# Performance work log

Hardware: AMD Instinct MI355X
Metric: run time of the kernel (lower is better)

## Reference

```python
import jax, jax.numpy as jnp
import numpy as np

NEG = -10000.0
SLOPE = 0.2


def setup_inputs() -> dict:
    key = jax.random.key(0)
    k1, k2, k3, k4, k5 = jax.random.split(key, 5)
    B, N, F_in, F_out = 8, 2048, 512, 512
    text = jax.random.normal(k1, (B, N, F_in), dtype=jnp.float32)
    adj = jax.random.randint(k2, (B, N, N), 0, 2, dtype=jnp.int32)
    sc = 1.0 / np.sqrt(F_in)
    W = jax.random.normal(k3, (F_in, F_out), dtype=jnp.float32) * sc
    b = jnp.zeros((F_out,), dtype=jnp.float32)
    a_src = jax.random.normal(k4, (F_out,), dtype=jnp.float32) * sc
    a_dst = jax.random.normal(k5, (F_out,), dtype=jnp.float32) * sc
    return {"text": text, "adj": adj, "W": W, "b": b, "a_src": a_src, "a_dst": a_dst}


def reference(text, adj, W, b, a_src, a_dst):
    # hidden: [B, N, F_out]
    hidden = jnp.einsum("bnf,fo->bno", text, W) + b
    s = jnp.einsum("bno,o->bn", hidden, a_src)  # src score per node
    d = jnp.einsum("bno,o->bn", hidden, a_dst)  # dst score per node
    scores = s[:, :, None] + d[:, None, :]      # [B, N, N]
    scores = jnp.where(scores >= 0, scores, SLOPE * scores)  # LeakyReLU
    # faithful to original: masked_fill where adj.bool() is True
    scores = jnp.where(adj.astype(bool), NEG, scores)
    attn = jax.nn.softmax(scores, axis=-1)
    return jnp.einsum("bnm,bmo->bno", attn, hidden)
```

## Files before the change

### kernel.cpp

```cpp
#include <hip/hip_runtime.h>
#include <stdint.h>

#define NB 8
#define NN 2048
#define NF 512
#define TOTN (NB * NN)

typedef unsigned short u16;
typedef short bf16x8 __attribute__((ext_vector_type(8)));
typedef float f32x4 __attribute__((ext_vector_type(4)));

__device__ __forceinline__ u16 f2bf(float x) {
  unsigned u = __float_as_uint(x);
  unsigned r = 0x7FFFu + ((u >> 16) & 1u);
  return (u16)((u + r) >> 16);
}

__device__ __forceinline__ void gl2lds16(const void* g, void* l) {
  __builtin_amdgcn_global_load_lds((const __attribute__((address_space(1))) void*)g,
                                   (__attribute__((address_space(3))) void*)l,
                                   16, 0, 0);
}


__global__ __launch_bounds__(256) void prep_kernel(
    const float* __restrict__ text, const float* __restrict__ W,
    const int* __restrict__ adj, u16* __restrict__ text_bf,
    u16* __restrict__ Wt, uint32_t* __restrict__ bm,
    float* __restrict__ sd) {
  int blk = blockIdx.x;
  if (blk < 8192) {
    int idx = blk * 256 + threadIdx.x;
    float4 v = ((const float4*)text)[idx];
    ushort4 o;
    o.x = f2bf(v.x); o.y = f2bf(v.y); o.z = f2bf(v.z); o.w = f2bf(v.w);
    ((ushort4*)text_bf)[idx] = o;
  } else if (blk < 9216) {
    int t = (blk - 8192) * 256 + threadIdx.x;
    int o = t >> 9, f = t & 511;
    Wt[o * NF + f] = f2bf(W[f * NF + o]);
  } else if (blk < 13312) {
    int gid = (blk - 9216) * 256 + threadIdx.x;
    const int4* p = (const int4*)(adj + (size_t)gid * 32);
    uint32_t bits = 0;
#pragma unroll
    for (int c = 0; c < 8; ++c) {
      int4 a = p[c];
      bits |= (uint32_t)(a.x != 0) << (c * 4 + 0);
      bits |= (uint32_t)(a.y != 0) << (c * 4 + 1);
      bits |= (uint32_t)(a.z != 0) << (c * 4 + 2);
      bits |= (uint32_t)(a.w != 0) << (c * 4 + 3);
    }
    bm[gid] = bits;
  } else {
    float4* p = (float4*)sd;
#pragma unroll
    for (int c = 0; c < 32; ++c)
      p[c * 256 + threadIdx.x] = (float4){0.f, 0.f, 0.f, 0.f};
  }
}

__global__ __launch_bounds__(256) void gemm1_kernel(
    const u16* __restrict__ A,
    const u16* __restrict__ Bt,
    const float* __restrict__ bias, const float* __restrict__ a_src,
    const float* __restrict__ a_dst, u16* __restrict__ hS,
    float* __restrict__ s, float* __restrict__ d) {
  __shared__ u16 Alds[128 * 32];
  __shared__ u16 Blds[128 * 32];

  const int bn = blockIdx.x, bm_ = blockIdx.y;
  const int t = threadIdx.x, wave = t >> 6, lane = t & 63;
  const int wm = (wave >> 1) * 64, wn = (wave & 1) * 64;

  f32x4 acc[4][4];
#pragma unroll
  for (int i = 0; i < 4; ++i)
#pragma unroll
    for (int j = 0; j < 4; ++j) acc[i][j] = (f32x4){0.f, 0.f, 0.f, 0.f};

  const int rowA0 = bm_ * 128, rowB0 = bn * 128;
  const int srow = (lane >> 2);
  const int scol = (lane & 3) * 8;

  for (int kt = 0; kt < NF; kt += 32) {
#pragma unroll
    for (int q = 0; q < 2; ++q) {
      int r = wave * 32 + q * 16;
      gl2lds16(A + (size_t)(rowA0 + r + srow) * NF + (kt + scol), &Alds[r * 32]);
    }
#pragma unroll
    for (int q = 0; q < 2; ++q) {
      int r = wave * 32 + q * 16;
      gl2lds16(Bt + (size_t)(rowB0 + r + srow) * NF + (kt + scol), &Blds[r * 32]);
    }
    __syncthreads();

    const int fr = lane & 15;
    const int k0 = (lane >> 4) * 8;
    bf16x8 af[4], bfr[4];
#pragma unroll
    for (int i = 0; i < 4; ++i)
      af[i] = *(const bf16x8*)&Alds[(wm + i * 16 + fr) * 32 + k0];
#pragma unroll
    for (int j = 0; j < 4; ++j)
      bfr[j] = *(const bf16x8*)&Blds[(wn + j * 16 + fr) * 32 + k0];
#pragma unroll
    for (int i = 0; i < 4; ++i)
#pragma unroll
      for (int j = 0; j < 4; ++j)
        acc[i][j] = __builtin_amdgcn_mfma_f32_16x16x32_bf16(af[i], bfr[j],
                                                            acc[i][j], 0, 0, 0);
    __syncthreads();
  }

  const int quad = lane >> 4, ln16 = lane & 15;
  float sa[4] = {0.f, 0.f, 0.f, 0.f}, da[4] = {0.f, 0.f, 0.f, 0.f};
#pragma unroll
  for (int i = 0; i < 4; ++i) {
    int m0 = bm_ * 128 + wm + i * 16 + quad * 4;
#pragma unroll
    for (int r = 0; r < 4; ++r) {
      int m = m0 + r;
      float bv = bias[m];
      float asv = a_src[m], adv = a_dst[m];
      int oh = m >> 8, och = (m >> 4) & 15, rc = m & 15;
#pragma unroll
      for (int j = 0; j < 4; ++j) {
        int n = bn * 128 + wn + j * 16 + ln16;
        float h = acc[i][j][r] + bv;
        int zz = n >> 11, nz = n & 2047;
        int kc = nz >> 5, kin = nz & 31;
        size_t off = ((((size_t)zz * 2 + oh) * 64 + kc) << 13)
                     + (och << 9)
                     + ((size_t)(rc * 4 + ((kin >> 3) ^ ((rc >> 1) & 3))) << 3)
                     + (kin & 7);
        hS[off] = f2bf(h);
        sa[j] = fmaf(h, asv, sa[j]);
        da[j] = fmaf(h, adv, da[j]);
      }
    }
  }
#pragma unroll
  for (int j = 0; j < 4; ++j) {
    float v = sa[j] + __shfl_xor(sa[j], 16, 64);
    v += __shfl_xor(v, 32, 64);
    float w2 = da[j] + __shfl_xor(da[j], 16, 64);
    w2 += __shfl_xor(w2, 32, 64);
    if (quad == 0) {
      int n = bn * 128 + wn + j * 16 + ln16;
      atomicAdd(&s[n], v);
      atomicAdd(&d[n], w2);
    }
  }
}

__global__ __launch_bounds__(256, 2) void fused_attn_kernel(
    const uint32_t* __restrict__ bm, const float* __restrict__ s,
    const float* __restrict__ d, const u16* __restrict__ hS,
    float* __restrict__ out) {
  __shared__ u16 Blds[2][16384];
  __shared__ u16 Plds[4096];
  __shared__ float lpart[256];
  __shared__ float linv_lds[64];

  const int z = blockIdx.z, oh = blockIdx.y;
  const int i0 = blockIdx.x * 64;
  const int t = threadIdx.x, wave = t >> 6, lane = t & 63;
  const int quad = lane >> 4, ln16 = lane & 15;

  const int pr = t >> 2;
  const int ko = (t & 3) * 16;
  const float si = s[z * NN + i0 + pr];
  const uint32_t* bmrow = bm + (size_t)(z * NN + i0 + pr) * 64;
  const float* db = d + z * NN;

  const char* slabB = (const char*)hS + (size_t)(z * 2 + oh) * 1048576;

  f32x4 acc[4][4];
#pragma unroll
  for (int i = 0; i < 4; ++i)
#pragma unroll
    for (int j = 0; j < 4; ++j) acc[i][j] = (f32x4){0.f, 0.f, 0.f, 0.f};

  const int fslot = ln16 * 4 + (quad ^ ((ln16 >> 1) & 3));
  const int prc = pr & 15, pch = pr >> 4;
  const int ph = ko >> 5, pq0 = (ko >> 3) & 3;
  char* pbase = (char*)Plds + ph * 4096 + pch * 1024;
  char* pdst0 = pbase + (prc * 4 + (pq0 ^ ((prc >> 1) & 3))) * 16;
  char* pdst1 = pbase + (prc * 4 + ((pq0 + 1) ^ ((prc >> 1) & 3))) * 16;

  uint32_t bw = bmrow[ko >> 5];
  float4 dv[4];
#pragma unroll
  for (int c = 0; c < 4; ++c) dv[c] = *(const float4*)&db[ko + c * 4];
  __builtin_amdgcn_sched_barrier(0);
#pragma unroll
  for (int c = 0; c < 8; ++c) {
    int boff = (c * 4 + wave) * 1024;
    gl2lds16(slabB + boff + lane * 16, (char*)&Blds[0][0] + boff);
  }

  float lsum = 0.f;
  int buf = 0;

  for (int kt = 0; kt < NN; kt += 64) {
    uint32_t bits16 = (bw >> (ko & 16)) & 0xFFFFu;
    u16 pk[16];
#pragma unroll
    for (int cc = 0; cc < 4; ++cc) {
      float4 dq = dv[cc];
#pragma unroll
      for (int e = 0; e < 4; ++e) {
        float dj = (e == 0) ? dq.x : (e == 1) ? dq.y : (e == 2) ? dq.z : dq.w;
        float x = si + dj;
        float xm = fmaxf(x, 0.2f * x);
        float p = ((bits16 >> (cc * 4 + e)) & 1u) ? 0.f : __expf(xm);
        lsum += p;
        pk[cc * 4 + e] = f2bf(p);
      }
    }

    bool more = (kt + 64 < NN);
    if (more) {
      bw = bmrow[((kt + 64) >> 5) + (ko >> 5)];
#pragma unroll
      for (int c = 0; c < 4; ++c)
        dv[c] = *(const float4*)&db[kt + 64 + ko + c * 4];
      __builtin_amdgcn_sched_barrier(0);
      const char* gB = slabB + (size_t)(kt + 64) * 512;
      char* bdst = (char*)&Blds[buf ^ 1][0];
#pragma unroll
      for (int c = 0; c < 8; ++c) {
        int boff = (c * 4 + wave) * 1024;
        gl2lds16(gB + boff + lane * 16, bdst + boff);
      }
    }

    *(int4*)pdst0 = *(int4*)&pk[0];
    *(int4*)pdst1 = *(int4*)&pk[8];

    if (more)
      asm volatile("s_waitcnt vmcnt(13) lgkmcnt(0)" ::: "memory");
    else
      asm volatile("s_waitcnt vmcnt(0) lgkmcnt(0)" ::: "memory");
    __builtin_amdgcn_s_barrier();
    asm volatile("" ::: "memory");

    const char* bbase = (const char*)&Blds[buf][0];
#pragma unroll
    for (int h = 0; h < 2; ++h) {
      bf16x8 af[4], bfv[4];
#pragma unroll
      for (int i = 0; i < 4; ++i)
        af[i] = *(const bf16x8*)((const char*)Plds + h * 4096 + i * 1024 + fslot * 16);
#pragma unroll
      for (int j = 0; j < 4; ++j)
        bfv[j] = *(const bf16x8*)(bbase + h * 16384 +
                                  (wave * 4 + j) * 1024 + fslot * 16);
#pragma unroll
      for (int i = 0; i < 4; ++i)
#pragma unroll
        for (int j = 0; j < 4; ++j)
          acc[i][j] = __builtin_amdgcn_mfma_f32_16x16x32_bf16(af[i], bfv[j],
                                                              acc[i][j], 0, 0, 0);
    }

    asm volatile("" ::: "memory");
    __builtin_amdgcn_s_barrier();
    asm volatile("" ::: "memory");
    buf ^= 1;
  }

  lpart[pr * 4 + (t & 3)] = lsum;
  __syncthreads();
  if (t < 64) {
    const float* lp = &lpart[t * 4];
    linv_lds[t] = 1.0f / ((lp[0] + lp[1]) + (lp[2] + lp[3]));
  }
  __syncthreads();

#pragma unroll
  for (int i = 0; i < 4; ++i) {
#pragma unroll
    for (int r = 0; r < 4; ++r) {
      int m = i * 16 + quad * 4 + r;
      float sc = linv_lds[m];
      float* ob = out + ((size_t)(z * NN) + i0 + m) * NF + oh * 256 + wave * 64;
#pragma unroll
      for (int j = 0; j < 4; ++j) ob[j * 16 + ln16] = acc[i][j][r] * sc;
    }
  }
}

extern "C" void kernel_launch(void* const* d_in, const int* in_sizes, int n_in,
                              void* d_out, int out_size, void* d_ws,
                              size_t ws_size, hipStream_t stream) {
  const float* text  = (const float*)d_in[0];
  const int*   adj   = (const int*)d_in[1];
  const float* W     = (const float*)d_in[2];
  const float* bias  = (const float*)d_in[3];
  const float* a_src = (const float*)d_in[4];
  const float* a_dst = (const float*)d_in[5];
  float* out = (float*)d_out;

  char* ws = (char*)d_ws;
  u16*      text_bf = (u16*)(ws + 0);
  u16*      Wt      = (u16*)(ws + 16777216);
  u16*      hS      = (u16*)(ws + 17301504);
  float*    s       = (float*)(ws + 34078720);
  float*    d       = (float*)(ws + 34144256);
  uint32_t* bmask   = (uint32_t*)(ws + 34209792);

  prep_kernel<<<13313, 256, 0, stream>>>(text, W, adj, text_bf, Wt, bmask, s);

  gemm1_kernel<<<dim3(128, 4, 1), 256, 0, stream>>>(Wt, text_bf, bias, a_src,
                                                    a_dst, hS, s, d);

  fused_attn_kernel<<<dim3(NN / 64, 2, NB), 256, 0, stream>>>(bmask, s, d, hS,
                                                              out);
}
```

Baseline: 299.0 us.

## Move adjacency bitmask packing into GEMM launch and reorder attention block mapping

Adjacency-to-bitmask packing moves from the prep kernel into extra blocks of the GEMM kernel, so the memory-bound adj read (128MB) can overlap with the compute-bound GEMM tiles instead of running serially before it. The attention kernel switches to a 1D grid whose lowest bits index the batch and output half. Consecutive blocks therefore hit different batches, which changes L2/MALL locality and the spread across XCDs. The GEMM blocks come first in the 1D grid, so the packing blocks may only fill in after them.

```diff
diff --git a/kernel.cpp b/kernel.cpp
--- a/kernel.cpp
+++ b/kernel.cpp
@@ -25,8 +25,7 @@
 
 __global__ __launch_bounds__(256) void prep_kernel(
     const float* __restrict__ text, const float* __restrict__ W,
-    const int* __restrict__ adj, u16* __restrict__ text_bf,
-    u16* __restrict__ Wt, uint32_t* __restrict__ bm,
+    u16* __restrict__ text_bf, u16* __restrict__ Wt,
     float* __restrict__ sd) {
   int blk = blockIdx.x;
   if (blk < 8192) {
@@ -39,8 +38,29 @@
     int t = (blk - 8192) * 256 + threadIdx.x;
     int o = t >> 9, f = t & 511;
     Wt[o * NF + f] = f2bf(W[f * NF + o]);
-  } else if (blk < 13312) {
-    int gid = (blk - 9216) * 256 + threadIdx.x;
+  } else {
+    float4* p = (float4*)sd;
+#pragma unroll
+    for (int c = 0; c < 32; ++c)
+      p[c * 256 + threadIdx.x] = (float4){0.f, 0.f, 0.f, 0.f};
+  }
+}
+
+__global__ __launch_bounds__(256) void gemm1_kernel(
+    const u16* __restrict__ A,
+    const u16* __restrict__ Bt,
+    const float* __restrict__ bias, const float* __restrict__ a_src,
+    const float* __restrict__ a_dst, const int* __restrict__ adj,
+    u16* __restrict__ hS, float* __restrict__ s, float* __restrict__ d,
+    uint32_t* __restrict__ bmout) {
+  __shared__ u16 Alds[128 * 32];
+  __shared__ u16 Blds[128 * 32];
+
+  const int bid = blockIdx.x;
+  const int t = threadIdx.x;
+
+  if (bid >= 512) {
+    int gid = (bid - 512) * 256 + t;
     const int4* p = (const int4*)(adj + (size_t)gid * 32);
     uint32_t bits = 0;
 #pragma unroll
@@ -51,26 +71,12 @@
       bits |= (uint32_t)(a.z != 0) << (c * 4 + 2);
       bits |= (uint32_t)(a.w != 0) << (c * 4 + 3);
     }
-    bm[gid] = bits;
-  } else {
-    float4* p = (float4*)sd;
-#pragma unroll
-    for (int c = 0; c < 32; ++c)
-      p[c * 256 + threadIdx.x] = (float4){0.f, 0.f, 0.f, 0.f};
-  }
-}
-
-__global__ __launch_bounds__(256) void gemm1_kernel(
-    const u16* __restrict__ A,
-    const u16* __restrict__ Bt,
-    const float* __restrict__ bias, const float* __restrict__ a_src,
-    const float* __restrict__ a_dst, u16* __restrict__ hS,
-    float* __restrict__ s, float* __restrict__ d) {
-  __shared__ u16 Alds[128 * 32];
-  __shared__ u16 Blds[128 * 32];
-
-  const int bn = blockIdx.x, bm_ = blockIdx.y;
-  const int t = threadIdx.x, wave = t >> 6, lane = t & 63;
+    bmout[gid] = bits;
+    return;
+  }
+
+  const int bn = bid & 127, bm_ = bid >> 7;
+  const int wave = t >> 6, lane = t & 63;
   const int wm = (wave >> 1) * 64, wn = (wave & 1) * 64;
 
   f32x4 acc[4][4];
@@ -164,8 +170,10 @@
   __shared__ float lpart[256];
   __shared__ float linv_lds[64];
 
-  const int z = blockIdx.z, oh = blockIdx.y;
-  const int i0 = blockIdx.x * 64;
+  const int bid = blockIdx.x;
+  const int z = bid & 7;
+  const int oh = (bid >> 3) & 1;
+  const int i0 = (bid >> 4) * 64;
   const int t = threadIdx.x, wave = t >> 6, lane = t & 63;
   const int quad = lane >> 4, ln16 = lane & 15;
 
@@ -312,11 +320,10 @@
   float*    d       = (float*)(ws + 34144256);
   uint32_t* bmask   = (uint32_t*)(ws + 34209792);
 
-  prep_kernel<<<13313, 256, 0, stream>>>(text, W, adj, text_bf, Wt, bmask, s);
-
-  gemm1_kernel<<<dim3(128, 4, 1), 256, 0, stream>>>(Wt, text_bf, bias, a_src,
-                                                    a_dst, hS, s, d);
-
-  fused_attn_kernel<<<dim3(NN / 64, 2, NB), 256, 0, stream>>>(bmask, s, d, hS,
-                                                              out);
-}
+  prep_kernel<<<9217, 256, 0, stream>>>(text, W, text_bf, Wt, s);
+
+  gemm1_kernel<<<4608, 256, 0, stream>>>(Wt, text_bf, bias, a_src, a_dst, adj,
+                                         hS, s, d, bmask);
+
+  fused_attn_kernel<<<512, 256, 0, stream>>>(bmask, s, d, hS, out);
+}
```

Result: no change. 296.4 us (-0.9%).
